# Optimization experiments

Measured on AMD Instinct MI355X. Metric: run time of the kernel, lower is better.

The kernel has to match this reference:

```python
import jax, jax.numpy as jnp
import numpy as np

B, SQ, SE, SI, SEI = 16, 512, 512, 256, 768
D, H = 1024, 16
DK = D // H
L1, L2 = 0.5, 0.5
NEG = -1e30  # stand-in for -inf masked_fill


def setup_inputs() -> dict:
    key = jax.random.key(0)
    ks = jax.random.split(key, 32)
    f = lambda i, shp: jax.random.normal(ks[i], shp, dtype=jnp.float32)
    w = lambda i: f(i, (D, D)) * (1.0 / np.sqrt(D))
    b = lambda i: jnp.zeros((D,), jnp.float32)
    inp = {
        'q': f(0, (B, SQ, D)),
        'k_e': f(1, (B, SE, D)), 'v_e': f(2, (B, SE, D)),
        'k_i': f(3, (B, SI, D)), 'v_i': f(4, (B, SI, D)),
        'k_ei': f(5, (B, SEI, D)), 'v_ei': f(6, (B, SEI, D)),
        'mask_e': jax.random.randint(ks[7], (B, SQ, SE), 0, 2) == 1,
        'mask_ei': jax.random.randint(ks[8], (B, SQ, SEI), 0, 2) == 1,
        'e_padding_mask': jax.random.randint(ks[9], (B, SE), 0, 2) == 1,
        'ei_padding_mask': jax.random.randint(ks[10], (B, SEI), 0, 2) == 1,
        'Wq': w(11), 'bq': b(11),
        'Wke': w(12), 'bke': b(12), 'Wve': w(13), 'bve': b(13),
        'Wki': w(14), 'bki': b(14), 'Wvi': w(15), 'bvi': b(15),
        'Wkei': w(16), 'bkei': b(16), 'Wvei': w(17), 'bvei': b(17),
        'Wout': w(18), 'bout': b(18),
    }
    return inp


def _proj(x, W, b):
    # (B, S, D) -> (B, H, S, DK)
    B_, S_, _ = x.shape
    return (x @ W + b).reshape(B_, S_, H, DK).transpose(0, 2, 1, 3)


def _attn(qh, kh, vh, mask, pad_mask):
    # qh: (B,H,Sq,DK), kh/vh: (B,H,Sk,DK)
    s = jnp.einsum('bhqd,bhkd->bhqk', qh, kh) / np.sqrt(DK)
    if mask is not None:
        s = jnp.where(mask[:, None, :, :], NEG, s)
    if pad_mask is not None:
        s = jnp.where(pad_mask[:, None, None, :], NEG, s)
    w = jax.nn.softmax(s, axis=-1)
    # dropout in original is applied to a discarded temp (eval / no-op)
    return jnp.einsum('bhqk,bhkd->bhqd', w, vh), w


def reference(q, k_e, k_i, k_ei, v_e, v_i, v_ei,
              mask_e, mask_ei, e_padding_mask, ei_padding_mask,
              Wq, bq, Wke, bke, Wve, bve, Wki, bki, Wvi, bvi,
              Wkei, bkei, Wvei, bvei, Wout, bout):
    qh = _proj(q, Wq, bq)
    o_e, aw_e = _attn(qh, _proj(k_e, Wke, bke), _proj(v_e, Wve, bve), mask_e, e_padding_mask)
    o_i, aw_i = _attn(qh, _proj(k_i, Wki, bki), _proj(v_i, Wvi, bvi), None, None)
    o_ei, _ = _attn(qh, _proj(k_ei, Wkei, bkei), _proj(v_ei, Wvei, bvei), mask_ei, ei_padding_mask)
    scores = o_e + L1 * o_i + L2 * o_ei  # (B,H,Sq,DK)
    concat = scores.transpose(0, 2, 1, 3).reshape(B, SQ, D)
    output = concat @ Wout + bout
    return output, aw_e, aw_i
```

## Files before the change

kernel.cpp:

```cpp
#include <hip/hip_runtime.h>
#include <stdint.h>

typedef __attribute__((ext_vector_type(8))) short bf16x8;
typedef __attribute__((ext_vector_type(4))) short s16x4;
typedef __attribute__((ext_vector_type(4))) float f32x4;

__device__ __forceinline__ short f2bf(float f){
  unsigned x = __float_as_uint(f);
  unsigned r = (x + 0x7fffu + ((x >> 16) & 1u)) >> 16;
  return (short)r;
}

__device__ __forceinline__ void g2l16(const void* g, void* l){
  __builtin_amdgcn_global_load_lds(
      (const __attribute__((address_space(1))) unsigned int*)(unsigned long long)(uintptr_t)g,
      (__attribute__((address_space(3))) unsigned int*)(unsigned int)(uintptr_t)l,
      16, 0, 0);
}

struct W8 { const float* w[8]; };
__global__ __launch_bounds__(256) void pack_w8(W8 ws8, short* __restrict__ out){
  const int m = blockIdx.y;
  const float scl = (m == 0) ? 0.125f : 1.0f;
  const float* __restrict__ W = ws8.w[m];
  short* o = out + (size_t)m * 1048576 + (size_t)blockIdx.x * 4096;
  const int kt = blockIdx.x & 31, nt = blockIdx.x >> 5;
  const int t = threadIdx.x;
  #pragma unroll
  for (int i = 0; i < 16; ++i){
    int flat = i * 256 + t;
    int kl = flat >> 7;
    int nl = flat & 127;
    o[nl * 32 + kl] = f2bf(W[(size_t)(kt * 32 + kl) * 1024 + nt * 128 + nl] * scl);
  }
}

struct GSeg { const short* A; const short* Wp; const float* bias; void* C;
              int om; int S; int mt; float bs; };
struct Big {
  GSeg g[4];
  const float* cin[4]; short* cout[4]; int n8[4];
  const int* me; const int* pe; unsigned* be;
  const int* mi; const int* pi; unsigned* bi;
  int act[8];
};

__device__ __forceinline__ void gemm_core(const GSeg sg,
                                          short (*sA)[4096], short (*sB)[4096]){
  if ((int)blockIdx.x >= sg.mt) return;
  const int t = threadIdx.x;
  const int m0 = blockIdx.x * 128;
  const int nt = blockIdx.y;
  const int n0 = nt * 128;
  const int w = t >> 6, lane = t & 63, lr = lane & 15, lg = lane >> 4;
  const int wm = (w >> 1) * 64, wn = (w & 1) * 64;

  const int arow  = t >> 2;
  const int acol8 = (t & 3) * 8;
  const short* Ag = sg.A + (size_t)(m0 + arow) * 1024 + acol8;
  const short* Bg = sg.Wp + (size_t)nt * 32 * 4096 + t * 8;

  f32x4 acc[4][4] = {};

  g2l16(Ag, sA[0] + t * 8);
  g2l16(Ag + 64 * 1024, sA[0] + 2048 + t * 8);
  g2l16(Bg, sB[0] + t * 8);
  g2l16(Bg + 2048, sB[0] + 2048 + t * 8);

  int cur = 0;
  for (int kt = 0; kt < 32; ++kt){
    __syncthreads();
    if (kt < 31){
      const int kn = kt + 1;
      g2l16(Ag + kn * 32, sA[cur ^ 1] + t * 8);
      g2l16(Ag + 64 * 1024 + kn * 32, sA[cur ^ 1] + 2048 + t * 8);
      const short* bt = Bg + (size_t)kn * 4096;
      g2l16(bt, sB[cur ^ 1] + t * 8);
      g2l16(bt + 2048, sB[cur ^ 1] + 2048 + t * 8);
    }

    bf16x8 af[4], bfr[4];
    #pragma unroll
    for (int mi = 0; mi < 4; ++mi)
      af[mi] = *(const bf16x8*)&sA[cur][(wm + mi * 16 + lr) * 32 + lg * 8];
    #pragma unroll
    for (int ni = 0; ni < 4; ++ni)
      bfr[ni] = *(const bf16x8*)&sB[cur][(wn + ni * 16 + lr) * 32 + lg * 8];
    #pragma unroll
    for (int mi = 0; mi < 4; ++mi)
      #pragma unroll
      for (int ni = 0; ni < 4; ++ni)
        acc[mi][ni] = __builtin_amdgcn_mfma_f32_16x16x32_bf16(
            af[mi], bfr[ni], acc[mi][ni], 0, 0, 0);
    cur ^= 1;
  }

  #pragma unroll
  for (int ni = 0; ni < 4; ++ni){
    const int n = n0 + wn + ni * 16 + lr;
    const float bv = sg.bias[n] * sg.bs;
    #pragma unroll
    for (int mi = 0; mi < 4; ++mi){
      const int mb = m0 + wm + mi * 16 + lg * 4;
      if (sg.om == 0){
        short* C = (short*)sg.C;
        #pragma unroll
        for (int j = 0; j < 4; ++j)
          C[(size_t)(mb + j) * 1024 + n] = f2bf(acc[mi][ni][j] + bv);
      } else if (sg.om == 1){
        short* C = (short*)sg.C;
        const int bb = mb / sg.S, sb = mb % sg.S;
        const int hh = n >> 6, dk = n & 63;
        s16x4 pk;
        #pragma unroll
        for (int j = 0; j < 4; ++j) pk[j] = f2bf(acc[mi][ni][j] + bv);
        *(s16x4*)&C[(((size_t)bb * 16 + hh) * 64 + dk) * sg.S + sb] = pk;
      } else {
        float* C = (float*)sg.C;
        #pragma unroll
        for (int j = 0; j < 4; ++j)
          C[(size_t)(mb + j) * 1024 + n] = acc[mi][ni][j] + bv;
      }
    }
  }
}

__device__ __forceinline__ void cvt_core(const float* __restrict__ in,
                                         short* __restrict__ out, int n8){
  const long long total = (long long)gridDim.x * gridDim.y * 256;
  for (long long i = (long long)(blockIdx.y * gridDim.x + blockIdx.x) * 256 + threadIdx.x;
       i < n8; i += total){
    const float4* p = (const float4*)in + i * 2;
    const float4 a = p[0], b = p[1];
    bf16x8 v;
    v[0] = f2bf(a.x); v[1] = f2bf(a.y); v[2] = f2bf(a.z); v[3] = f2bf(a.w);
    v[4] = f2bf(b.x); v[5] = f2bf(b.y); v[6] = f2bf(b.z); v[7] = f2bf(b.w);
    *(bf16x8*)(out + i * 8) = v;
  }
}

__device__ __forceinline__ void bits_core(const int* __restrict__ mask,
                                          const int* __restrict__ pad,
                                          unsigned* __restrict__ bits,
                                          int SK, int nsb, int nunits){
  const int nb = gridDim.x * gridDim.y;
  for (int u = blockIdx.y * gridDim.x + blockIdx.x; u < nunits; u += nb){
    const int row = u / nsb, sb = u - row * nsb;
    const int s = sb * 256 + threadIdx.x;
    const int b = row >> 9;
    const bool v = (mask[(size_t)row * SK + s] != 0) || (pad[(size_t)b * SK + s] != 0);
    unsigned long long bal = __ballot(v);
    const int lane = threadIdx.x & 63;
    if ((lane & 31) == 0)
      bits[((size_t)row * SK + s) >> 5] = (unsigned)(bal >> (lane & 32));
  }
}

__global__ __launch_bounds__(256) void mixk(Big big){
  __shared__ short sA[2][4096];
  __shared__ short sB[2][4096];
  const int a = big.act[blockIdx.z];
  if (a < 4)       gemm_core(big.g[a], sA, sB);
  else if (a < 8)  cvt_core(big.cin[a - 4], big.cout[a - 4], big.n8[a - 4]);
  else if (a == 8) bits_core(big.me, big.pe, big.be, 512, 2, 16384);
  else             bits_core(big.mi, big.pi, big.bi, 768, 3, 24576);
}

template<int SK, bool HAS_BIAS, bool SINGLE>
__device__ __forceinline__ void attn_mod(
    const short* __restrict__ Kp, const short* __restrict__ Vt,
    const unsigned* __restrict__ bits, float* __restrict__ aw,
    const bf16x8 (&qf)[2], f32x4 (&tot)[4], float wgt,
    short* sK, short* sV, short* sPw,
    int b, int h, int qw, int w, int lane, int lr, int lg){
  constexpr int NT  = SK / 128;
  constexpr int SKW = SK / 32;
  static_assert((NT & 1) == 0, "buffer-parity argument needs even NT");

  const int kchunk = (lane & 7) ^ ((lane >> 3) & 7);
  const short* Ksrc = Kp + ((size_t)b * SK + w * 16 + (lane >> 3)) * 1024 + h * 64 + kchunk * 8;
  const short* Vsrc = Vt + ((size_t)(b * 16 + h)) * 64 * SK;
  const int ldoff = w * 1024 + lane * 8;

  const unsigned* bitrow[4];
  if (HAS_BIAS){
    #pragma unroll
    for (int j = 0; j < 4; ++j)
      bitrow[j] = bits + ((size_t)(b * 512 + qw + lg * 4 + j)) * SKW;
  }

  float lrow[4];
  #pragma unroll
  for (int j = 0; j < 4; ++j) lrow[j] = 0.f;
  f32x4 acco[4] = {};

#define SKB(c) (sK + (c) * 8192)
#define SVB(c) (sV + (c) * 8192)
#define STAGE_K(c, s0) do{ \
    g2l16(Ksrc + (size_t)(s0) * 1024, SKB(c) + ldoff); \
    g2l16(Ksrc + (size_t)((s0) + 8) * 1024, SKB(c) + ldoff + 512); }while(0)
#define STAGE_V(c, s0) do{ \
    const int dd0 = w * 8 + (lane >> 4); \
    const int cg0 = (lane & 15) ^ (dd0 & 15); \
    g2l16(Vsrc + (size_t)dd0 * SK + (s0) + cg0 * 8, SVB(c) + ldoff); \
    const int dd1 = dd0 + 4; \
    const int cg1 = (lane & 15) ^ (dd1 & 15); \
    g2l16(Vsrc + (size_t)dd1 * SK + (s0) + cg1 * 8, SVB(c) + ldoff + 512); }while(0)

  if (!SINGLE){
    STAGE_K(0, 0);
    int cur = 0;
    for (int tt = 0; tt < NT; ++tt){
      __syncthreads();
      if (tt + 1 < NT) STAGE_K(cur ^ 1, (tt + 1) * 128);
      const short* kb = SKB(cur);

      f32x4 accs[8];
      #pragma unroll
      for (int si = 0; si < 8; ++si){
        f32x4 a = {};
        #pragma unroll
        for (int dt = 0; dt < 2; ++dt){
          bf16x8 kf = *(const bf16x8*)&kb[(si * 16 + lr) * 64 + ((dt * 4 + lg) ^ (lr & 7)) * 8];
          a = __builtin_amdgcn_mfma_f32_16x16x32_bf16(qf[dt], kf, a, 0, 0, 0);
        }
        accs[si] = a;
      }

      #pragma unroll
      for (int j = 0; j < 4; ++j){
        unsigned wb[4];
        if (HAS_BIAS){
          #pragma unroll
          for (int sp = 0; sp < 4; ++sp) wb[sp] = bitrow[j][tt * 4 + sp];
        }
        float ssum = 0.f;
        #pragma unroll
        for (int si = 0; si < 8; ++si){
          float v = accs[si][j];
          if (HAS_BIAS && ((wb[si >> 1] >> ((si & 1) * 16 + lr)) & 1u)) v = -1e30f;
          ssum += __expf(v);
        }
        lrow[j] += ssum;
      }
      cur ^= 1;
    }

    #pragma unroll
    for (int j = 0; j < 4; ++j){
      #pragma unroll
      for (int d = 1; d < 16; d <<= 1) lrow[j] += __shfl_xor(lrow[j], d);
    }
    float rinv[4];
    #pragma unroll
    for (int j = 0; j < 4; ++j) rinv[j] = lrow[j] > 0.f ? 1.0f / lrow[j] : 0.f;

    STAGE_K(0, 0);
    STAGE_V(0, 0);
    cur = 0;
    for (int tt = 0; tt < NT; ++tt){
      const int s0 = tt * 128;
      __syncthreads();
      if (tt + 1 < NT){ STAGE_K(cur ^ 1, s0 + 128); STAGE_V(cur ^ 1, s0 + 128); }
      const short* kb = SKB(cur);
      const short* vb = SVB(cur);

      f32x4 accs[8];
      #pragma unroll
      for (int si = 0; si < 8; ++si){
        f32x4 a = {};
        #pragma unroll
        for (int dt = 0; dt < 2; ++dt){
          bf16x8 kf = *(const bf16x8*)&kb[(si * 16 + lr) * 64 + ((dt * 4 + lg) ^ (lr & 7)) * 8];
          a = __builtin_amdgcn_mfma_f32_16x16x32_bf16(qf[dt], kf, a, 0, 0, 0);
        }
        accs[si] = a;
      }

      #pragma unroll
      for (int half = 0; half < 2; ++half){
        #pragma unroll
        for (int j = 0; j < 4; ++j){
          unsigned wb[2];
          if (HAS_BIAS){
            #pragma unroll
            for (int sp = 0; sp < 2; ++sp) wb[sp] = bitrow[j][tt * 4 + half * 2 + sp];
          }
          const int qq = lg * 4 + j;
          float* awrow = aw + (((size_t)(b * 16 + h)) * 512 + qw + qq) * SK + s0 + half * 64 + lr;
          #pragma unroll
          for (int si2 = 0; si2 < 4; ++si2){
            const int si = half * 4 + si2;
            float v = accs[si][j];
            if (HAS_BIAS && ((wb[si2 >> 1] >> ((si2 & 1) * 16 + lr)) & 1u)) v = -1e30f;
            const float p = __expf(v) * rinv[j];
            __builtin_nontemporal_store(p, &awrow[si2 * 16]);
            sPw[qq * 64 + (((si2 * 2 + (lr >> 3)) ^ (qq & 7)) * 8) + (lr & 7)] = f2bf(p);
          }
        }
        #pragma unroll
        for (int kt2 = 0; kt2 < 2; ++kt2){
          const int kt = half * 2 + kt2;
          bf16x8 pa = *(const bf16x8*)&sPw[lr * 64 + (((kt2 * 4 + lg) ^ (lr & 7)) * 8)];
          #pragma unroll
          for (int ni = 0; ni < 4; ++ni){
            bf16x8 vf = *(const bf16x8*)&vb[(ni * 16 + lr) * 128 + ((kt * 4 + lg) ^ lr) * 8];
            acco[ni] = __builtin_amdgcn_mfma_f32_16x16x32_bf16(pa, vf, acco[ni], 0, 0, 0);
          }
        }
      }
      cur ^= 1;
    }

    #pragma unroll
    for (int ni = 0; ni < 4; ++ni)
      #pragma unroll
      for (int j = 0; j < 4; ++j)
        tot[ni][j] += wgt * acco[ni][j];
  } else {
    STAGE_K(0, 0);
    STAGE_V(0, 0);
    int cur = 0;
    for (int tt = 0; tt < NT; ++tt){
      const int s0 = tt * 128;
      __syncthreads();
      if (tt + 1 < NT){ STAGE_K(cur ^ 1, s0 + 128); STAGE_V(cur ^ 1, s0 + 128); }
      const short* kb = SKB(cur);
      const short* vb = SVB(cur);

      f32x4 accs[8];
      #pragma unroll
      for (int si = 0; si < 8; ++si){
        f32x4 a = {};
        #pragma unroll
        for (int dt = 0; dt < 2; ++dt){
          bf16x8 kf = *(const bf16x8*)&kb[(si * 16 + lr) * 64 + ((dt * 4 + lg) ^ (lr & 7)) * 8];
          a = __builtin_amdgcn_mfma_f32_16x16x32_bf16(qf[dt], kf, a, 0, 0, 0);
        }
        accs[si] = a;
      }

      #pragma unroll
      for (int half = 0; half < 2; ++half){
        #pragma unroll
        for (int j = 0; j < 4; ++j){
          unsigned wb[2];
          if (HAS_BIAS){
            #pragma unroll
            for (int sp = 0; sp < 2; ++sp) wb[sp] = bitrow[j][tt * 4 + half * 2 + sp];
          }
          const int qq = lg * 4 + j;
          float ls = 0.f;
          #pragma unroll
          for (int si2 = 0; si2 < 4; ++si2){
            const int si = half * 4 + si2;
            float v = accs[si][j];
            if (HAS_BIAS && ((wb[si2 >> 1] >> ((si2 & 1) * 16 + lr)) & 1u)) v = -1e30f;
            const float p = __expf(v);
            ls += p;
            sPw[qq * 64 + (((si2 * 2 + (lr >> 3)) ^ (qq & 7)) * 8) + (lr & 7)] = f2bf(p);
          }
          lrow[j] += ls;
        }
        #pragma unroll
        for (int kt2 = 0; kt2 < 2; ++kt2){
          const int kt = half * 2 + kt2;
          bf16x8 pa = *(const bf16x8*)&sPw[lr * 64 + (((kt2 * 4 + lg) ^ (lr & 7)) * 8)];
          #pragma unroll
          for (int ni = 0; ni < 4; ++ni){
            bf16x8 vf = *(const bf16x8*)&vb[(ni * 16 + lr) * 128 + ((kt * 4 + lg) ^ lr) * 8];
            acco[ni] = __builtin_amdgcn_mfma_f32_16x16x32_bf16(pa, vf, acco[ni], 0, 0, 0);
          }
        }
      }
      cur ^= 1;
    }

    #pragma unroll
    for (int j = 0; j < 4; ++j){
      #pragma unroll
      for (int d = 1; d < 16; d <<= 1) lrow[j] += __shfl_xor(lrow[j], d);
      const float r = lrow[j] > 0.f ? wgt / lrow[j] : 0.f;
      #pragma unroll
      for (int ni = 0; ni < 4; ++ni) tot[ni][j] += r * acco[ni][j];
    }
  }
#undef SKB
#undef SVB
#undef STAGE_K
#undef STAGE_V
}

__global__ __launch_bounds__(512)
void attn_fused(const short* __restrict__ Qp,
                const short* __restrict__ Kep, const short* __restrict__ Vte,
                const unsigned* __restrict__ bits_e, float* __restrict__ aw_e,
                const short* __restrict__ Kip, const short* __restrict__ Vti,
                float* __restrict__ aw_i,
                const short* __restrict__ Keip, const short* __restrict__ Vtei,
                const unsigned* __restrict__ bits_ei,
                short* __restrict__ concat){
  __shared__ short sK[2 * 8192];
  __shared__ short sV[2 * 8192];
  __shared__ short sP[8192];

  const int bid = blockIdx.x;
  const int qt = bid >> 8;
  const int g  = bid & 255;
  const int h = g & 15, b = g >> 4;
  const int q0 = qt * 128;
  const int t = threadIdx.x, w = t >> 6, lane = t & 63;
  const int lr = lane & 15, lg = lane >> 4;
  const int qw = q0 + w * 16;
  short* sPw = sP + w * 1024;

  const short* Qb = Qp + ((size_t)(b * 512 + qw + lr)) * 1024 + h * 64;
  bf16x8 qf[2];
  qf[0] = *(const bf16x8*)&Qb[lg * 8];
  qf[1] = *(const bf16x8*)&Qb[32 + lg * 8];

  f32x4 tot[4] = {};

  attn_mod<512, true , false>(Kep,  Vte,  bits_e,  aw_e, qf, tot, 1.0f,
                              sK, sV, sPw, b, h, qw, w, lane, lr, lg);
  attn_mod<256, false, false>(Kip,  Vti,  nullptr, aw_i, qf, tot, 0.5f,
                              sK, sV, sPw, b, h, qw, w, lane, lr, lg);
  attn_mod<768, true , true >(Keip, Vtei, bits_ei, nullptr, qf, tot, 0.5f,
                              sK, sV, sPw, b, h, qw, w, lane, lr, lg);

  #pragma unroll
  for (int ni = 0; ni < 4; ++ni)
    #pragma unroll
    for (int j = 0; j < 4; ++j){
      const size_t addr = ((size_t)(b * 512 + qw + lg * 4 + j)) * 1024 + h * 64 + ni * 16 + lr;
      concat[addr] = f2bf(tot[ni][j]);
    }
}

extern "C" void kernel_launch(void* const* d_in, const int* in_sizes, int n_in,
                              void* d_out, int out_size, void* d_ws, size_t ws_size,
                              hipStream_t stream){
  const float* q    = (const float*)d_in[0];
  const float* k_e  = (const float*)d_in[1];
  const float* v_e  = (const float*)d_in[2];
  const float* k_i  = (const float*)d_in[3];
  const float* v_i  = (const float*)d_in[4];
  const float* k_ei = (const float*)d_in[5];
  const float* v_ei = (const float*)d_in[6];
  const int* mask_e  = (const int*)d_in[7];
  const int* mask_ei = (const int*)d_in[8];
  const int* pad_e   = (const int*)d_in[9];
  const int* pad_ei  = (const int*)d_in[10];
  const float* Wq   = (const float*)d_in[11]; const float* bq   = (const float*)d_in[12];
  const float* Wke  = (const float*)d_in[13]; const float* bke  = (const float*)d_in[14];
  const float* Wve  = (const float*)d_in[15]; const float* bve  = (const float*)d_in[16];
  const float* Wki  = (const float*)d_in[17]; const float* bki  = (const float*)d_in[18];
  const float* Wvi  = (const float*)d_in[19]; const float* bvi  = (const float*)d_in[20];
  const float* Wkei = (const float*)d_in[21]; const float* bkei = (const float*)d_in[22];
  const float* Wvei = (const float*)d_in[23]; const float* bvei = (const float*)d_in[24];
  const float* Wout = (const float*)d_in[25]; const float* bout = (const float*)d_in[26];

  char* ws = (char*)d_ws;
  const size_t MB = 1048576;
  short* PW   = (short*)(ws);
  short* StA0 = (short*)(ws + 16 * MB);
  short* StA1 = (short*)(ws + 32 * MB);
  short* StA2 = (short*)(ws + 48 * MB);
  short* Kip  = (short*)(ws + 16 * MB);
  short* Vti  = (short*)(ws + 24 * MB);
  short* Keip = (short*)(ws + 32 * MB);
  unsigned* bits_e  = (unsigned*)(ws + 56 * MB);
  unsigned* bits_ei = (unsigned*)(ws + 58 * MB);
  short* StB0 = (short*)(ws + 64 * MB);
  short* StB1 = (short*)(ws + 72 * MB);
  short* StC0 = (short*)(ws + 80 * MB);
  short* StC1 = (short*)(ws + 104 * MB);
  short* concat = (short*)(ws + 64 * MB);
  short* Qp   = (short*)(ws + 128 * MB);
  short* Kep  = (short*)(ws + 144 * MB);
  short* Vte  = (short*)(ws + 160 * MB);
  short* Vtei = (short*)(ws + 176 * MB);

  float* out0 = (float*)d_out;
  float* aw_e = out0 + 8388608;
  float* aw_i = out0 + 75497472;

  W8 w8;
  w8.w[0] = Wq;  w8.w[1] = Wke;  w8.w[2] = Wve;  w8.w[3] = Wki;
  w8.w[4] = Wvi; w8.w[5] = Wkei; w8.w[6] = Wvei; w8.w[7] = Wout;
  pack_w8<<<dim3(256, 8), 256, 0, stream>>>(w8, PW);

  Big bg{};
  bg.me = mask_e;  bg.pe = pad_e;  bg.be = bits_e;
  bg.mi = mask_ei; bg.pi = pad_ei; bg.bi = bits_ei;

  {
    Big c = bg;
    c.cin[0] = q;   c.cout[0] = StA0; c.n8[0] = 1048576;
    c.cin[1] = k_e; c.cout[1] = StA1; c.n8[1] = 1048576;
    c.cin[2] = v_e; c.cout[2] = StA2; c.n8[2] = 1048576;
    c.act[0] = 4; c.act[1] = 5; c.act[2] = 6;
    mixk<<<dim3(96, 8, 3), 256, 0, stream>>>(c);
  }
  {
    Big c = bg;
    c.g[0] = {StA0, PW + 0 * 1048576, bq,  Qp,  0, 512, 64, 0.125f};
    c.g[1] = {StA1, PW + 1 * 1048576, bke, Kep, 0, 512, 64, 1.0f};
    c.g[2] = {StA2, PW + 2 * 1048576, bve, Vte, 1, 512, 64, 1.0f};
    c.cin[0] = k_i;  c.cout[0] = StB0; c.n8[0] = 524288;
    c.cin[1] = v_i;  c.cout[1] = StB1; c.n8[1] = 524288;
    c.cin[2] = k_ei; c.cout[2] = StC0; c.n8[2] = 1572864;
    c.cin[3] = v_ei; c.cout[3] = StC1; c.n8[3] = 1572864;
    c.act[0] = 0; c.act[1] = 1; c.act[2] = 2;
    c.act[3] = 4; c.act[4] = 5; c.act[5] = 6; c.act[6] = 7;
    mixk<<<dim3(96, 8, 7), 256, 0, stream>>>(c);
  }
  {
    Big c = bg;
    c.g[0] = {StB0, PW + 3 * 1048576, bki,  Kip,  0, 256, 32, 1.0f};
    c.g[1] = {StB1, PW + 4 * 1048576, bvi,  Vti,  1, 256, 32, 1.0f};
    c.g[2] = {StC0, PW + 5 * 1048576, bkei, Keip, 0, 768, 96, 1.0f};
    c.g[3] = {StC1, PW + 6 * 1048576, bvei, Vtei, 1, 768, 96, 1.0f};
    c.act[0] = 0; c.act[1] = 1; c.act[2] = 2; c.act[3] = 3;
    c.act[4] = 8; c.act[5] = 9;
    mixk<<<dim3(96, 8, 6), 256, 0, stream>>>(c);
  }

  attn_fused<<<1024, 512, 0, stream>>>(Qp, Kep, Vte, bits_e, aw_e,
                                       Kip, Vti, aw_i, Keip, Vtei, bits_ei, concat);

  {
    Big c = bg;
    c.g[0] = {concat, PW + 7 * 1048576, bout, out0, 2, 512, 64, 1.0f};
    c.act[0] = 0;
    mixk<<<dim3(64, 8, 1), 256, 0, stream>>>(c);
  }
}
```

Measured before the change: 523.6 us.

## Interleave aux and GEMM blocks in flat grids and add MFMA priority hints

Replaces the z-indexed mixed launcher with flat 1D grids where every ninth block does conversion or mask-bit packing and the rest do GEMM tiles. Idle padded blocks (mt checks) are gone, and memory-bound work is spread across the GEMM blocks. Adds s_setprio around MFMA loops in the GEMM and attention kernels, and moves the row-sum reduction after the K/V staging issue so it overlaps the loads. The added risk is index-mapping complexity and an uneven mix of aux and GEMM work.

```diff
diff --git a/kernel.cpp b/kernel.cpp
--- a/kernel.cpp
+++ b/kernel.cpp
@@ -36,29 +36,21 @@
 }
 
 struct GSeg { const short* A; const short* Wp; const float* bias; void* C;
-              int om; int S; int mt; float bs; };
-struct Big {
-  GSeg g[4];
-  const float* cin[4]; short* cout[4]; int n8[4];
-  const int* me; const int* pe; unsigned* be;
-  const int* mi; const int* pi; unsigned* bi;
-  int act[8];
-};
+              int om; int S; float bs; };
 
 __device__ __forceinline__ void gemm_core(const GSeg sg,
-                                          short (*sA)[4096], short (*sB)[4096]){
-  if ((int)blockIdx.x >= sg.mt) return;
+                                          short (*sA)[4096], short (*sB)[4096],
+                                          int bx, int by){
   const int t = threadIdx.x;
-  const int m0 = blockIdx.x * 128;
-  const int nt = blockIdx.y;
-  const int n0 = nt * 128;
+  const int m0 = bx * 128;
+  const int n0 = by * 128;
   const int w = t >> 6, lane = t & 63, lr = lane & 15, lg = lane >> 4;
   const int wm = (w >> 1) * 64, wn = (w & 1) * 64;
 
   const int arow  = t >> 2;
   const int acol8 = (t & 3) * 8;
   const short* Ag = sg.A + (size_t)(m0 + arow) * 1024 + acol8;
-  const short* Bg = sg.Wp + (size_t)nt * 32 * 4096 + t * 8;
+  const short* Bg = sg.Wp + (size_t)by * 32 * 4096 + t * 8;
 
   f32x4 acc[4][4] = {};
 
@@ -86,12 +78,14 @@
     #pragma unroll
     for (int ni = 0; ni < 4; ++ni)
       bfr[ni] = *(const bf16x8*)&sB[cur][(wn + ni * 16 + lr) * 32 + lg * 8];
+    __builtin_amdgcn_s_setprio(1);
     #pragma unroll
     for (int mi = 0; mi < 4; ++mi)
       #pragma unroll
       for (int ni = 0; ni < 4; ++ni)
         acc[mi][ni] = __builtin_amdgcn_mfma_f32_16x16x32_bf16(
             af[mi], bfr[ni], acc[mi][ni], 0, 0, 0);
+    __builtin_amdgcn_s_setprio(0);
     cur ^= 1;
   }
 
@@ -126,10 +120,10 @@
 }
 
 __device__ __forceinline__ void cvt_core(const float* __restrict__ in,
-                                         short* __restrict__ out, int n8){
-  const long long total = (long long)gridDim.x * gridDim.y * 256;
-  for (long long i = (long long)(blockIdx.y * gridDim.x + blockIdx.x) * 256 + threadIdx.x;
-       i < n8; i += total){
+                                         short* __restrict__ out, int n8,
+                                         int local, int nb){
+  const long long stride = (long long)nb * 256;
+  for (long long i = (long long)local * 256 + threadIdx.x; i < n8; i += stride){
     const float4* p = (const float4*)in + i * 2;
     const float4 a = p[0], b = p[1];
     bf16x8 v;
@@ -142,9 +136,9 @@
 __device__ __forceinline__ void bits_core(const int* __restrict__ mask,
                                           const int* __restrict__ pad,
                                           unsigned* __restrict__ bits,
-                                          int SK, int nsb, int nunits){
-  const int nb = gridDim.x * gridDim.y;
-  for (int u = blockIdx.y * gridDim.x + blockIdx.x; u < nunits; u += nb){
+                                          int SK, int nsb, int nunits,
+                                          int local, int nb){
+  for (int u = local; u < nunits; u += nb){
     const int row = u / nsb, sb = u - row * nsb;
     const int s = sb * 256 + threadIdx.x;
     const int b = row >> 9;
@@ -156,14 +150,60 @@
   }
 }
 
-__global__ __launch_bounds__(256) void mixk(Big big){
+struct Mix {
+  GSeg g[4];
+  const float* cin[4]; short* cout[4]; int n8[4];
+  const int* me; const int* pe; unsigned* be;
+  const int* mi; const int* pi; unsigned* bi;
+};
+
+template<int MODE>
+__global__ __launch_bounds__(256) void mix2(Mix mx, int ngemm){
   __shared__ short sA[2][4096];
   __shared__ short sB[2][4096];
-  const int a = big.act[blockIdx.z];
-  if (a < 4)       gemm_core(big.g[a], sA, sB);
-  else if (a < 8)  cvt_core(big.cin[a - 4], big.cout[a - 4], big.n8[a - 4]);
-  else if (a == 8) bits_core(big.me, big.pe, big.be, 512, 2, 16384);
-  else             bits_core(big.mi, big.pi, big.bi, 768, 3, 24576);
+  const int bid = blockIdx.x;
+  const int aux = (bid % 9) == 8;
+  if (aux){
+    const int aid = bid / 9;
+    if (MODE == 0){
+      if (aid < 24)       cvt_core(mx.cin[0], mx.cout[0], mx.n8[0], aid,        24);
+      else if (aid < 48)  cvt_core(mx.cin[1], mx.cout[1], mx.n8[1], aid - 24,   24);
+      else if (aid < 120) cvt_core(mx.cin[2], mx.cout[2], mx.n8[2], aid - 48,   72);
+      else                cvt_core(mx.cin[3], mx.cout[3], mx.n8[3], aid - 120,  72);
+    } else {
+      if (aid < 128) bits_core(mx.me, mx.pe, mx.be, 512, 2, 16384, aid,       128);
+      else           bits_core(mx.mi, mx.pi, mx.bi, 768, 3, 24576, aid - 128, 128);
+    }
+    return;
+  }
+  const int gid = bid - (bid + 1) / 9;
+  if (gid >= ngemm) return;
+  int seg, bx, by;
+  if (MODE == 0){
+    seg = gid >> 9;
+    const int r = gid & 511;
+    bx = r & 63; by = r >> 6;
+  } else {
+    if (gid < 512){
+      const int xx = gid & 63, my = gid >> 6;
+      seg = xx >> 5; bx = xx & 31; by = my;
+    } else {
+      const int r = gid - 512;
+      const int xx = r % 192, my = r / 192;
+      seg = 2 + xx / 96; bx = xx % 96; by = my;
+    }
+  }
+  gemm_core(mx.g[seg], sA, sB, bx, by);
+}
+
+__global__ __launch_bounds__(256) void cvt3(Mix mx){
+  cvt_core(mx.cin[blockIdx.z], mx.cout[blockIdx.z], mx.n8[blockIdx.z],
+           blockIdx.x, gridDim.x);
+}
+__global__ __launch_bounds__(256) void gemm1(Mix mx){
+  __shared__ short sA[2][4096];
+  __shared__ short sB[2][4096];
+  gemm_core(mx.g[0], sA, sB, blockIdx.x, blockIdx.y);
 }
 
 template<int SK, bool HAS_BIAS, bool SINGLE>
@@ -216,6 +256,7 @@
       const short* kb = SKB(cur);
 
       f32x4 accs[8];
+      __builtin_amdgcn_s_setprio(1);
       #pragma unroll
       for (int si = 0; si < 8; ++si){
         f32x4 a = {};
@@ -226,6 +267,7 @@
         }
         accs[si] = a;
       }
+      __builtin_amdgcn_s_setprio(0);
 
       #pragma unroll
       for (int j = 0; j < 4; ++j){
@@ -246,17 +288,18 @@
       cur ^= 1;
     }
 
-    #pragma unroll
-    for (int j = 0; j < 4; ++j){
-      #pragma unroll
-      for (int d = 1; d < 16; d <<= 1) lrow[j] += __shfl_xor(lrow[j], d);
-    }
-    float rinv[4];
-    #pragma unroll
-    for (int j = 0; j < 4; ++j) rinv[j] = lrow[j] > 0.f ? 1.0f / lrow[j] : 0.f;
-
     STAGE_K(0, 0);
     STAGE_V(0, 0);
+
+    #pragma unroll
+    for (int j = 0; j < 4; ++j){
+      #pragma unroll
+      for (int d = 1; d < 16; d <<= 1) lrow[j] += __shfl_xor(lrow[j], d);
+    }
+    float rinv[4];
+    #pragma unroll
+    for (int j = 0; j < 4; ++j) rinv[j] = lrow[j] > 0.f ? 1.0f / lrow[j] : 0.f;
+
     cur = 0;
     for (int tt = 0; tt < NT; ++tt){
       const int s0 = tt * 128;
@@ -266,6 +309,7 @@
       const short* vb = SVB(cur);
 
       f32x4 accs[8];
+      __builtin_amdgcn_s_setprio(1);
       #pragma unroll
       for (int si = 0; si < 8; ++si){
         f32x4 a = {};
@@ -276,6 +320,7 @@
         }
         accs[si] = a;
       }
+      __builtin_amdgcn_s_setprio(0);
 
       #pragma unroll
       for (int half = 0; half < 2; ++half){
@@ -298,6 +343,7 @@
             sPw[qq * 64 + (((si2 * 2 + (lr >> 3)) ^ (qq & 7)) * 8) + (lr & 7)] = f2bf(p);
           }
         }
+        __builtin_amdgcn_s_setprio(1);
         #pragma unroll
         for (int kt2 = 0; kt2 < 2; ++kt2){
           const int kt = half * 2 + kt2;
@@ -308,6 +354,7 @@
             acco[ni] = __builtin_amdgcn_mfma_f32_16x16x32_bf16(pa, vf, acco[ni], 0, 0, 0);
           }
         }
+        __builtin_amdgcn_s_setprio(0);
       }
       cur ^= 1;
     }
@@ -329,6 +376,7 @@
       const short* vb = SVB(cur);
 
       f32x4 accs[8];
+      __builtin_amdgcn_s_setprio(1);
       #pragma unroll
       for (int si = 0; si < 8; ++si){
         f32x4 a = {};
@@ -339,6 +387,7 @@
         }
         accs[si] = a;
       }
+      __builtin_amdgcn_s_setprio(0);
 
       #pragma unroll
       for (int half = 0; half < 2; ++half){
@@ -362,6 +411,7 @@
           }
           lrow[j] += ls;
         }
+        __builtin_amdgcn_s_setprio(1);
         #pragma unroll
         for (int kt2 = 0; kt2 < 2; ++kt2){
           const int kt = half * 2 + kt2;
@@ -372,6 +422,7 @@
             acco[ni] = __builtin_amdgcn_mfma_f32_16x16x32_bf16(pa, vf, acco[ni], 0, 0, 0);
           }
         }
+        __builtin_amdgcn_s_setprio(0);
       }
       cur ^= 1;
     }
@@ -490,49 +541,43 @@
   w8.w[4] = Wvi; w8.w[5] = Wkei; w8.w[6] = Wvei; w8.w[7] = Wout;
   pack_w8<<<dim3(256, 8), 256, 0, stream>>>(w8, PW);
 
-  Big bg{};
+  Mix bg{};
   bg.me = mask_e;  bg.pe = pad_e;  bg.be = bits_e;
   bg.mi = mask_ei; bg.pi = pad_ei; bg.bi = bits_ei;
 
   {
-    Big c = bg;
+    Mix c = bg;
     c.cin[0] = q;   c.cout[0] = StA0; c.n8[0] = 1048576;
     c.cin[1] = k_e; c.cout[1] = StA1; c.n8[1] = 1048576;
     c.cin[2] = v_e; c.cout[2] = StA2; c.n8[2] = 1048576;
-    c.act[0] = 4; c.act[1] = 5; c.act[2] = 6;
-    mixk<<<dim3(96, 8, 3), 256, 0, stream>>>(c);
+    cvt3<<<dim3(768, 1, 3), 256, 0, stream>>>(c);
   }
   {
-    Big c = bg;
-    c.g[0] = {StA0, PW + 0 * 1048576, bq,  Qp,  0, 512, 64, 0.125f};
-    c.g[1] = {StA1, PW + 1 * 1048576, bke, Kep, 0, 512, 64, 1.0f};
-    c.g[2] = {StA2, PW + 2 * 1048576, bve, Vte, 1, 512, 64, 1.0f};
+    Mix c = bg;
+    c.g[0] = {StA0, PW + 0 * 1048576, bq,  Qp,  0, 512, 0.125f};
+    c.g[1] = {StA1, PW + 1 * 1048576, bke, Kep, 0, 512, 1.0f};
+    c.g[2] = {StA2, PW + 2 * 1048576, bve, Vte, 1, 512, 1.0f};
     c.cin[0] = k_i;  c.cout[0] = StB0; c.n8[0] = 524288;
     c.cin[1] = v_i;  c.cout[1] = StB1; c.n8[1] = 524288;
     c.cin[2] = k_ei; c.cout[2] = StC0; c.n8[2] = 1572864;
     c.cin[3] = v_ei; c.cout[3] = StC1; c.n8[3] = 1572864;
-    c.act[0] = 0; c.act[1] = 1; c.act[2] = 2;
-    c.act[3] = 4; c.act[4] = 5; c.act[5] = 6; c.act[6] = 7;
-    mixk<<<dim3(96, 8, 7), 256, 0, stream>>>(c);
+    mix2<0><<<1728, 256, 0, stream>>>(c, 1536);
   }
   {
-    Big c = bg;
-    c.g[0] = {StB0, PW + 3 * 1048576, bki,  Kip,  0, 256, 32, 1.0f};
-    c.g[1] = {StB1, PW + 4 * 1048576, bvi,  Vti,  1, 256, 32, 1.0f};
-    c.g[2] = {StC0, PW + 5 * 1048576, bkei, Keip, 0, 768, 96, 1.0f};
-    c.g[3] = {StC1, PW + 6 * 1048576, bvei, Vtei, 1, 768, 96, 1.0f};
-    c.act[0] = 0; c.act[1] = 1; c.act[2] = 2; c.act[3] = 3;
-    c.act[4] = 8; c.act[5] = 9;
-    mixk<<<dim3(96, 8, 6), 256, 0, stream>>>(c);
+    Mix c = bg;
+    c.g[0] = {StB0, PW + 3 * 1048576, bki,  Kip,  0, 256, 1.0f};
+    c.g[1] = {StB1, PW + 4 * 1048576, bvi,  Vti,  1, 256, 1.0f};
+    c.g[2] = {StC0, PW + 5 * 1048576, bkei, Keip, 0, 768, 1.0f};
+    c.g[3] = {StC1, PW + 6 * 1048576, bvei, Vtei, 1, 768, 1.0f};
+    mix2<1><<<2304, 256, 0, stream>>>(c, 2048);
   }
 
   attn_fused<<<1024, 512, 0, stream>>>(Qp, Kep, Vte, bits_e, aw_e,
                                        Kip, Vti, aw_i, Keip, Vtei, bits_ei, concat);
 
   {
-    Big c = bg;
-    c.g[0] = {concat, PW + 7 * 1048576, bout, out0, 2, 512, 64, 1.0f};
-    c.act[0] = 0;
-    mixk<<<dim3(64, 8, 1), 256, 0, stream>>>(c);
-  }
-}
+    Mix c = bg;
+    c.g[0] = {concat, PW + 7 * 1048576, bout, out0, 2, 512, 1.0f};
+    gemm1<<<dim3(64, 8), 256, 0, stream>>>(c);
+  }
+}
```

After: 682.5 us. 1.3x slower.
